# Kernel tuning notes

Measured on AMD Instinct MI355X. Metric: run time of the kernel, lower is better.

## Reference

```python
import jax, jax.numpy as jnp
import numpy as np

NUM_CLASSES = 50000
NUM_INSTANCE = 2
FEAT_LEN = 256
SELECTION = 0.7
N_PROPOSALS = 1024
QUEUE_SIZE = NUM_CLASSES * NUM_INSTANCE


def setup_inputs() -> dict:
    key = jax.random.key(0)
    k1, k2 = jax.random.split(key)
    features = jax.random.normal(k1, (N_PROPOSALS, FEAT_LEN), dtype=jnp.float32)
    pid_labels = jax.random.randint(k2, (N_PROPOSALS,), 0, NUM_CLASSES)
    large_batch_queue = jnp.zeros((QUEUE_SIZE, FEAT_LEN), dtype=jnp.float32)
    queue_label = jnp.zeros((QUEUE_SIZE,), dtype=jnp.float32)
    return {"features": features, "pid_labels": pid_labels,
            "large_batch_queue": large_batch_queue, "queue_label": queue_label}


def _forward(features, pid_labels, queue, qlabel):
    n = pid_labels.shape[0]
    qsize = queue.shape[0]
    # torch.unique returns sorted uniques; pad with -1 which fails the
    # 0 <= label < num_classes check and is therefore a no-op step.
    uniq = jnp.unique(pid_labels, size=n, fill_value=-1)

    def step(state, inp):
        queue, qlabel, tail, judge = state
        indx, label = inp
        feat = features[indx]  # NOTE: indexed by enumerate index, as in the original
        # queue[label] is a single row -> matmul is a dot product; max of scalar = scalar
        score = jnp.dot(queue[label], feat)
        cond = ((score < SELECTION) & (judge == 1)) | (judge == 0)
        valid = (label >= 0) & (label < NUM_CLASSES)
        write = valid & cond
        queue = queue.at[tail].set(jnp.where(write, feat, queue[tail]))
        qlabel = qlabel.at[tail].set(jnp.where(write, label.astype(qlabel.dtype), qlabel[tail]))
        tail = tail + write.astype(tail.dtype)
        wrap = tail >= qsize
        tail = jnp.where(wrap, tail - qsize, tail)
        judge = jnp.where(wrap, jnp.int32(1), judge)
        return (queue, qlabel, tail, judge), None

    init = (queue, qlabel, jnp.array(0, jnp.int32), jnp.array(0, jnp.int32))
    (queue, qlabel, _, _), _ = jax.lax.scan(step, init, (jnp.arange(n, dtype=jnp.int32), uniq))
    return queue, qlabel


def reference(features, pid_labels, large_batch_queue, queue_label):
    return _forward(features, pid_labels, large_batch_queue, queue_label)
```

## Files before the change

### kernel.cpp

```cpp
#include <hip/hip_runtime.h>

#define QSIZE    100000
#define FEAT     256
#define NPROP    1024
#define NCLASS   50000
#define NWORDS   1563

#define NB_MAIN  6250
#define NB_FIX   64
#define NB_LAB   98

typedef float fvec4 __attribute__((ext_vector_type(4)));

__global__ __launch_bounds__(1024)
void unique_kernel(const int* __restrict__ labels, int n,
                   float* __restrict__ uniq_ws, int* __restrict__ U_ws) {
    __shared__ unsigned bm[NWORDS];
    __shared__ int wsum[16];
    __shared__ int wbase[16];
    const int tid = threadIdx.x;

    for (int w = tid; w < NWORDS; w += 1024) bm[w] = 0u;
    __syncthreads();

    if (tid < n) {
        const int L = labels[tid];
        atomicOr(&bm[L >> 5], 1u << (L & 31));
    }
    __syncthreads();

    const int b0 = 2 * tid;
    unsigned w0 = 0u, w1 = 0u;
    int c = 0;
    if (b0 < NWORDS)     { w0 = bm[b0];     c += __popc(w0); }
    if (b0 + 1 < NWORDS) { w1 = bm[b0 + 1]; c += __popc(w1); }

    const int lane = tid & 63, wave = tid >> 6;
    int sc = c;
    for (int off = 1; off < 64; off <<= 1) {
        int o = __shfl_up(sc, off, 64);
        if (lane >= off) sc += o;
    }
    if (lane == 63) wsum[wave] = sc;
    __syncthreads();

    if (tid == 0) {
        int acc = 0;
        for (int i = 0; i < 16; ++i) { wbase[i] = acc; acc += wsum[i]; }
        *U_ws = acc;
    }
    __syncthreads();

    int pos = wbase[wave] + (sc - c);
    while (w0) {
        int b = __ffs(w0) - 1; w0 &= w0 - 1;
        uniq_ws[pos++] = (float)(b0 * 32 + b);
    }
    while (w1) {
        int b = __ffs(w1) - 1; w1 &= w1 - 1;
        uniq_ws[pos++] = (float)((b0 + 1) * 32 + b);
    }
}

__global__ __launch_bounds__(256)
void assemble_kernel(const fvec4* __restrict__ feat4,
                     const fvec4* __restrict__ qin4,
                     const float* __restrict__ qlab_in,
                     const float* __restrict__ uniq_ws,
                     const int*   __restrict__ U_ws,
                     fvec4* __restrict__ out0,
                     float* __restrict__ out1) {
    const int b = blockIdx.x;
    const int tid = threadIdx.x;

    if (b < NB_MAIN) {
        const int base = b * 1024 + tid;
        if (b < NB_FIX) {
            const int U = *U_ws;
            #pragma unroll
            for (int k = 0; k < 4; ++k) {
                const int i = base + k * 256;
                const int row = i >> 6;
                const fvec4 f = feat4[i];
                const fvec4 q = qin4[i];
                __builtin_nontemporal_store(row < U ? f : q, &out0[i]);
            }
        } else {
            fvec4 v0 = qin4[base];
            fvec4 v1 = qin4[base + 256];
            fvec4 v2 = qin4[base + 512];
            fvec4 v3 = qin4[base + 768];
            __builtin_nontemporal_store(v0, &out0[base]);
            __builtin_nontemporal_store(v1, &out0[base + 256]);
            __builtin_nontemporal_store(v2, &out0[base + 512]);
            __builtin_nontemporal_store(v3, &out0[base + 768]);
        }
    } else {
        const int b2 = b - NB_MAIN;
        const int base = b2 * 1024 + tid;
        if (b2 == 0) {
            const int U = *U_ws;
            #pragma unroll
            for (int k = 0; k < 4; ++k) {
                const int j = base + k * 256;
                const float u = uniq_ws[j];
                const float q = qlab_in[j];
                __builtin_nontemporal_store(j < U ? u : q, &out1[j]);
            }
        } else {
            #pragma unroll
            for (int k = 0; k < 4; ++k) {
                const int j = base + k * 256;
                if (j < QSIZE)
                    __builtin_nontemporal_store(qlab_in[j], &out1[j]);
            }
        }
    }
}

extern "C" void kernel_launch(void* const* d_in, const int* in_sizes, int n_in,
                              void* d_out, int out_size, void* d_ws, size_t ws_size,
                              hipStream_t stream) {
    const float* features   = (const float*)d_in[0];
    const int*   pid_labels = (const int*)d_in[1];
    const float* queue_in   = (const float*)d_in[2];
    const float* qlabel_in  = (const float*)d_in[3];
    const int n = in_sizes[1];

    float* out0 = (float*)d_out;
    float* out1 = out0 + (size_t)QSIZE * FEAT;

    float* uniq_ws = (float*)d_ws;
    int*   U_ws    = (int*)((char*)d_ws + NPROP * sizeof(float));

    unique_kernel<<<1, NPROP, 0, stream>>>(pid_labels, n, uniq_ws, U_ws);
    assemble_kernel<<<NB_MAIN + NB_LAB, 256, 0, stream>>>(
        (const fvec4*)features, (const fvec4*)queue_in, qlabel_in,
        uniq_ws, U_ws, (fvec4*)out0, out1);
}
```

Before: 35.07 us.

## Fuse unique-label kernel into assemble kernel with per-block redundant bitmap

Removes the separate single-block unique kernel and its workspace round-trip. Each of the 64 feature-fix blocks now rebuilds the label bitmap in shared memory to get the unique count, and the label-fix block computes the sorted uniques locally into LDS. This drops one kernel launch and the serialization between launches. In exchange, the bitmap work is duplicated across 65 blocks and every block now reserves about 10KB of LDS, which may reduce occupancy for the bulk copy blocks.

After: 30.13 us. 14.1% less time.

```diff
diff --git a/kernel.cpp b/kernel.cpp
--- a/kernel.cpp
+++ b/kernel.cpp
@@ -1,10 +1,10 @@
 #include <hip/hip_runtime.h>
 
 #define QSIZE    100000
-#define FEAT     256
 #define NPROP    1024
 #define NCLASS   50000
 #define NWORDS   1563
+#define WPT      7
 
 #define NB_MAIN  6250
 #define NB_FIX   64
@@ -12,78 +12,51 @@
 
 typedef float fvec4 __attribute__((ext_vector_type(4)));
 
-__global__ __launch_bounds__(1024)
-void unique_kernel(const int* __restrict__ labels, int n,
-                   float* __restrict__ uniq_ws, int* __restrict__ U_ws) {
+__global__ __launch_bounds__(256)
+void fused_kernel(const fvec4* __restrict__ feat4,
+                  const fvec4* __restrict__ qin4,
+                  const float* __restrict__ qlab_in,
+                  const int*   __restrict__ labels,
+                  int n,
+                  fvec4* __restrict__ out0,
+                  float* __restrict__ out1) {
     __shared__ unsigned bm[NWORDS];
-    __shared__ int wsum[16];
-    __shared__ int wbase[16];
-    const int tid = threadIdx.x;
+    __shared__ float lds_u[NPROP];
+    __shared__ int wsum[4];
+    __shared__ int Ush;
 
-    for (int w = tid; w < NWORDS; w += 1024) bm[w] = 0u;
-    __syncthreads();
-
-    if (tid < n) {
-        const int L = labels[tid];
-        atomicOr(&bm[L >> 5], 1u << (L & 31));
-    }
-    __syncthreads();
-
-    const int b0 = 2 * tid;
-    unsigned w0 = 0u, w1 = 0u;
-    int c = 0;
-    if (b0 < NWORDS)     { w0 = bm[b0];     c += __popc(w0); }
-    if (b0 + 1 < NWORDS) { w1 = bm[b0 + 1]; c += __popc(w1); }
-
-    const int lane = tid & 63, wave = tid >> 6;
-    int sc = c;
-    for (int off = 1; off < 64; off <<= 1) {
-        int o = __shfl_up(sc, off, 64);
-        if (lane >= off) sc += o;
-    }
-    if (lane == 63) wsum[wave] = sc;
-    __syncthreads();
-
-    if (tid == 0) {
-        int acc = 0;
-        for (int i = 0; i < 16; ++i) { wbase[i] = acc; acc += wsum[i]; }
-        *U_ws = acc;
-    }
-    __syncthreads();
-
-    int pos = wbase[wave] + (sc - c);
-    while (w0) {
-        int b = __ffs(w0) - 1; w0 &= w0 - 1;
-        uniq_ws[pos++] = (float)(b0 * 32 + b);
-    }
-    while (w1) {
-        int b = __ffs(w1) - 1; w1 &= w1 - 1;
-        uniq_ws[pos++] = (float)((b0 + 1) * 32 + b);
-    }
-}
-
-__global__ __launch_bounds__(256)
-void assemble_kernel(const fvec4* __restrict__ feat4,
-                     const fvec4* __restrict__ qin4,
-                     const float* __restrict__ qlab_in,
-                     const float* __restrict__ uniq_ws,
-                     const int*   __restrict__ U_ws,
-                     fvec4* __restrict__ out0,
-                     float* __restrict__ out1) {
-    const int b = blockIdx.x;
+    const int b   = blockIdx.x;
     const int tid = threadIdx.x;
 
     if (b < NB_MAIN) {
         const int base = b * 1024 + tid;
         if (b < NB_FIX) {
-            const int U = *U_ws;
+            fvec4 f[4], q[4];
+            #pragma unroll
+            for (int k = 0; k < 4; ++k) {
+                f[k] = feat4[base + k * 256];
+                q[k] = qin4[base + k * 256];
+            }
+            for (int w = tid; w < NWORDS; w += 256) bm[w] = 0u;
+            if (tid == 0) Ush = 0;
+            __syncthreads();
+            for (int j = tid; j < n; j += 256) {
+                const int L = labels[j];
+                atomicOr(&bm[L >> 5], 1u << (L & 31));
+            }
+            __syncthreads();
+            int c = 0;
+            for (int w = tid; w < NWORDS; w += 256) c += __popc(bm[w]);
+            #pragma unroll
+            for (int off = 32; off; off >>= 1) c += __shfl_down(c, off, 64);
+            if ((tid & 63) == 0) atomicAdd(&Ush, c);
+            __syncthreads();
+            const int U = Ush;
             #pragma unroll
             for (int k = 0; k < 4; ++k) {
                 const int i = base + k * 256;
                 const int row = i >> 6;
-                const fvec4 f = feat4[i];
-                const fvec4 q = qin4[i];
-                __builtin_nontemporal_store(row < U ? f : q, &out0[i]);
+                __builtin_nontemporal_store(row < U ? f[k] : q[k], &out0[i]);
             }
         } else {
             fvec4 v0 = qin4[base];
@@ -97,20 +70,50 @@
         }
     } else {
         const int b2 = b - NB_MAIN;
-        const int base = b2 * 1024 + tid;
         if (b2 == 0) {
-            const int U = *U_ws;
+            for (int w = tid; w < NWORDS; w += 256) bm[w] = 0u;
+            __syncthreads();
+            for (int j = tid; j < n; j += 256) {
+                const int L = labels[j];
+                atomicOr(&bm[L >> 5], 1u << (L & 31));
+            }
+            __syncthreads();
+            const int w0   = tid * WPT;
+            const int wend = (w0 + WPT < NWORDS) ? (w0 + WPT) : NWORDS;
+            int c = 0;
+            for (int w = w0; w < wend; ++w) c += __popc(bm[w]);
+            const int lane = tid & 63, wv = tid >> 6;
+            int sc = c;
+            for (int off = 1; off < 64; off <<= 1) {
+                const int o = __shfl_up(sc, off, 64);
+                if (lane >= off) sc += o;
+            }
+            if (lane == 63) wsum[wv] = sc;
+            __syncthreads();
+            int wb = 0;
+            for (int i = 0; i < wv; ++i) wb += wsum[i];
+            const int U = wsum[0] + wsum[1] + wsum[2] + wsum[3];
+            int pos = wb + (sc - c);
+            for (int w = w0; w < wend; ++w) {
+                unsigned bits = bm[w];
+                while (bits) {
+                    const int bb = __ffs(bits) - 1; bits &= bits - 1;
+                    lds_u[pos++] = (float)(w * 32 + bb);
+                }
+            }
+            __syncthreads();
             #pragma unroll
             for (int k = 0; k < 4; ++k) {
-                const int j = base + k * 256;
-                const float u = uniq_ws[j];
-                const float q = qlab_in[j];
-                __builtin_nontemporal_store(j < U ? u : q, &out1[j]);
+                const int j = tid + k * 256;
+                const float u = lds_u[j];
+                const float ql = qlab_in[j];
+                __builtin_nontemporal_store(j < U ? u : ql, &out1[j]);
             }
         } else {
+            const int basej = b2 * 1024 + tid;
             #pragma unroll
             for (int k = 0; k < 4; ++k) {
-                const int j = base + k * 256;
+                const int j = basej + k * 256;
                 if (j < QSIZE)
                     __builtin_nontemporal_store(qlab_in[j], &out1[j]);
             }
@@ -128,13 +131,9 @@
     const int n = in_sizes[1];
 
     float* out0 = (float*)d_out;
-    float* out1 = out0 + (size_t)QSIZE * FEAT;
+    float* out1 = out0 + (size_t)QSIZE * 256;
 
-    float* uniq_ws = (float*)d_ws;
-    int*   U_ws    = (int*)((char*)d_ws + NPROP * sizeof(float));
-
-    unique_kernel<<<1, NPROP, 0, stream>>>(pid_labels, n, uniq_ws, U_ws);
-    assemble_kernel<<<NB_MAIN + NB_LAB, 256, 0, stream>>>(
+    fused_kernel<<<NB_MAIN + NB_LAB, 256, 0, stream>>>(
         (const fvec4*)features, (const fvec4*)queue_in, qlabel_in,
-        uniq_ws, U_ws, (fvec4*)out0, out1);
+        pid_labels, n, (fvec4*)out0, out1);
 }
```
